# Performance work log

Hardware: AMD Instinct MI355X
Metric: run time of the kernel (lower is better)

The kernel has to match this reference:

```python
import jax, jax.numpy as jnp
import numpy as np

B, D, E, TOP_K = 16384, 2048, 8, 2


def setup_inputs() -> dict:
    key = jax.random.key(0)
    ks = jax.random.split(key, 5)
    scale = 1.0 / np.sqrt(D)
    x = jax.random.normal(ks[0], (B, D), dtype=jnp.float32)
    # expert Linear(D, D) weights/biases, stacked over experts
    expert_w = jax.random.uniform(ks[1], (E, D, D), minval=-scale, maxval=scale, dtype=jnp.float32)
    expert_b = jax.random.uniform(ks[2], (E, D), minval=-scale, maxval=scale, dtype=jnp.float32)
    # gate Linear(D, E)
    gate_w = jax.random.uniform(ks[3], (D, E), minval=-scale, maxval=scale, dtype=jnp.float32)
    gate_b = jax.random.uniform(ks[4], (E,), minval=-scale, maxval=scale, dtype=jnp.float32)
    return {"x": x, "expert_w": expert_w, "expert_b": expert_b, "gate_w": gate_w, "gate_b": gate_b}


def reference(x, expert_w, expert_b, gate_w, gate_b):
    # gate logits: (B, E)
    logits = x @ gate_w + gate_b
    topk_logits, topk_idx = jax.lax.top_k(logits, TOP_K)          # (B, K)
    topk_weights = jax.nn.softmax(topk_logits, axis=-1)           # (B, K)
    # dense: compute every expert for every token (faithful to original)
    expert_outputs = jax.nn.relu(
        jnp.einsum("bd,edf->bef", x, expert_w) + expert_b[None, :, :]
    )                                                             # (B, E, D); dropout is identity in eval mode
    # gather the top-k experts per token
    selected = jnp.take_along_axis(expert_outputs, topk_idx[:, :, None], axis=1)  # (B, K, D)
    out = jnp.sum(selected * topk_weights[:, :, None], axis=1)    # (B, D)
    return out
```

## Files before the change

kernel.cpp:

```cpp
#include <hip/hip_runtime.h>
#include <hip/hip_bf16.h>
#include <math.h>

#define NB 16384
#define DD 2048
#define NE 8
#define TM 256
#define TN 256
#define BK 64
#define NKT (DD / BK)
#define MT_PER_PASS (NB / TM + NE)
#define NT_TILES (DD / TN)
#define GEMM_GRID (MT_PER_PASS * NT_TILES)

typedef float f32x4 __attribute__((ext_vector_type(4)));
typedef short bf16x8 __attribute__((ext_vector_type(8)));

__device__ __forceinline__ short f2bf(float f) {
  union { float f; unsigned u; } v; v.f = f;
  unsigned r = (v.u + 0x7FFFu + ((v.u >> 16) & 1u)) >> 16;
  return (short)r;
}

__device__ __forceinline__ void gload16(const void* g, void* l) {
  __builtin_amdgcn_global_load_lds((const __attribute__((address_space(1))) void*)g,
                                   (__attribute__((address_space(3))) void*)l,
                                   16, 0, 0);
}

__global__ void conv_wT(const float* __restrict__ w, short* __restrict__ wt) {
  __shared__ float tile[64][68];
  int bid = blockIdx.x;
  int e = bid >> 10;
  int tt = bid & 1023;
  int d0 = (tt >> 5) << 6;
  int f0 = (tt & 31) << 6;
  const float* we = w + (size_t)e * DD * DD;
  int t = threadIdx.x;
  int col = (t & 15) << 2;
#pragma unroll
  for (int p = 0; p < 4; ++p) {
    int dl = (t >> 4) + p * 16;
    f32x4 v = *(const f32x4*)(we + (size_t)(d0 + dl) * DD + f0 + col);
    *(f32x4*)&tile[dl][col] = v;
  }
  __syncthreads();
  int fl = t >> 2;
  int ds = (t & 3) << 4;
  short tmp[16];
#pragma unroll
  for (int j = 0; j < 16; ++j) tmp[j] = f2bf(tile[ds + j][fl]);
  short* dst = wt + (size_t)e * DD * DD + (size_t)(f0 + fl) * DD + d0 + ds;
  *(bf16x8*)dst = *(const bf16x8*)tmp;
  *(bf16x8*)(dst + 8) = *(const bf16x8*)(tmp + 8);
}

__global__ void gate_conv(const float* __restrict__ x, const float* __restrict__ gw,
                          const float* __restrict__ gb, short* __restrict__ xb,
                          int* __restrict__ ridx, float* __restrict__ rw) {
  int wid = threadIdx.x >> 6;
  int lane = threadIdx.x & 63;
  int b = blockIdx.x * 4 + wid;
  const float* xr = x + (size_t)b * DD;
  short* xbr = xb + (size_t)b * DD;
  double acc[8];
#pragma unroll
  for (int e = 0; e < 8; ++e) acc[e] = 0.0;
#pragma unroll
  for (int it = 0; it < 4; ++it) {
    int d8 = (it * 64 + lane) * 8;
    f32x4 a = *(const f32x4*)(xr + d8);
    f32x4 c = *(const f32x4*)(xr + d8 + 4);
    bf16x8 o;
    o[0] = f2bf(a[0]); o[1] = f2bf(a[1]); o[2] = f2bf(a[2]); o[3] = f2bf(a[3]);
    o[4] = f2bf(c[0]); o[5] = f2bf(c[1]); o[6] = f2bf(c[2]); o[7] = f2bf(c[3]);
    *(bf16x8*)(xbr + d8) = o;
#pragma unroll
    for (int j = 0; j < 8; ++j) {
      float xv = (j < 4) ? a[j] : c[j - 4];
      double xd = (double)xv;
      f32x4 g0 = *(const f32x4*)(gw + (size_t)(d8 + j) * 8);
      f32x4 g1 = *(const f32x4*)(gw + (size_t)(d8 + j) * 8 + 4);
      acc[0] += xd * g0[0]; acc[1] += xd * g0[1];
      acc[2] += xd * g0[2]; acc[3] += xd * g0[3];
      acc[4] += xd * g1[0]; acc[5] += xd * g1[1];
      acc[6] += xd * g1[2]; acc[7] += xd * g1[3];
    }
  }
#pragma unroll
  for (int off = 32; off > 0; off >>= 1) {
#pragma unroll
    for (int e = 0; e < 8; ++e) acc[e] += __shfl_down(acc[e], off);
  }
  if (lane == 0) {
    double l[8];
#pragma unroll
    for (int e = 0; e < 8; ++e) l[e] = acc[e] + (double)gb[e];
    int i0 = 0;
#pragma unroll
    for (int e = 1; e < 8; ++e) if (l[e] > l[i0]) i0 = e;
    int i1 = (i0 == 0) ? 1 : 0;
#pragma unroll
    for (int e = 0; e < 8; ++e) if (e != i0 && l[e] > l[i1]) i1 = e;
    double z = exp(l[i1] - l[i0]);
    float w0 = (float)(1.0 / (1.0 + z));
    float w1 = (float)(z / (1.0 + z));
    ridx[2 * b] = i0; ridx[2 * b + 1] = i1;
    rw[2 * b] = w0;   rw[2 * b + 1] = w1;
  }
}

__global__ void hist_tok(const int* __restrict__ ridx, int* __restrict__ partials) {
  __shared__ int h[16];
  int t = threadIdx.x;
  if (t < 16) h[t] = 0;
  __syncthreads();
  int t0 = blockIdx.x * 512;
  for (int i = t; i < 512; i += 256) {
    int tok = t0 + i;
    atomicAdd(&h[ridx[2 * tok]], 1);
    atomicAdd(&h[8 + ridx[2 * tok + 1]], 1);
  }
  __syncthreads();
  if (t < 16) partials[blockIdx.x * 16 + t] = h[t];
}

__global__ void scan_small(const int* __restrict__ partials, int* __restrict__ base,
                           int* __restrict__ cnts, int* __restrict__ offs) {
  __shared__ int c[16], o[16];
  int j = threadIdx.x;
  if (j < 16) {
    int s = 0;
    for (int b = 0; b < 32; ++b) s += partials[b * 16 + j];
    c[j] = s; cnts[j] = s;
  }
  __syncthreads();
  if (j < 2) {
    int a = 0;
    for (int e = 0; e < 8; ++e) { o[j * 8 + e] = a; a += c[j * 8 + e]; }
  }
  __syncthreads();
  if (j < 16) {
    int r = o[j];
    offs[j] = o[j];
    for (int b = 0; b < 32; ++b) { base[b * 16 + j] = r; r += partials[b * 16 + j]; }
  }
}

__global__ void scatter_tok(const int* __restrict__ ridx, const float* __restrict__ rw,
                            const int* __restrict__ base,
                            int* __restrict__ lists0, float* __restrict__ elw0,
                            int* __restrict__ lists1, float* __restrict__ elw1) {
  __shared__ int h[16];
  int t = threadIdx.x;
  if (t < 16) h[t] = 0;
  __syncthreads();
  int t0 = blockIdx.x * 512;
  const int* bb = base + blockIdx.x * 16;
  for (int i = t; i < 512; i += 256) {
    int tok = t0 + i;
    int e0 = ridx[2 * tok], e1 = ridx[2 * tok + 1];
    int r0 = atomicAdd(&h[e0], 1);
    int r1 = atomicAdd(&h[8 + e1], 1);
    int p0 = bb[e0] + r0;
    int p1 = bb[8 + e1] + r1;
    lists0[p0] = tok; elw0[p0] = rw[2 * tok];
    lists1[p1] = tok; elw1[p1] = rw[2 * tok + 1];
  }
}

#define VMCNT0 asm volatile("s_waitcnt vmcnt(0)" ::: "memory")

template <int ADD>
__global__ __launch_bounds__(512, 2)
void moe_gemm(const short* __restrict__ xb, const short* __restrict__ wt,
              const float* __restrict__ eb, const int* __restrict__ cnts,
              const int* __restrict__ offs, const int* __restrict__ lists,
              const float* __restrict__ elw, float* __restrict__ out) {
  __shared__ short As[2 * 16384];
  __shared__ short Bs[2 * 16384];

  int nt = blockIdx.x & 7;
  int mt = blockIdx.x >> 3;

  int e = 0, cnt = 0;
  for (; e < NE; ++e) {
    cnt = cnts[e];
    int te = (cnt + TM - 1) >> 8;
    if (mt < te) break;
    mt -= te;
  }
  if (e >= NE) return;

  int m0 = mt * TM;
  int n0 = nt * TN;
  int off_e = offs[e];
  int tid = threadIdx.x;
  int lane = tid & 63, wid = tid >> 6;
  int wr = wid >> 2, wc = wid & 3;

  int trow = tid >> 3;
  int scol = ((tid & 7) ^ (trow & 7)) << 3;
  const short* aptr[4];
  const short* bptr[4];
#pragma unroll
  for (int l = 0; l < 4; ++l) {
    int r = l * 64 + trow;
    int gr = m0 + r;
    int tok = lists[off_e + ((gr < cnt) ? gr : (cnt - 1))];
    aptr[l] = xb + (size_t)tok * DD + scol;
    bptr[l] = wt + ((size_t)e * DD + (size_t)(n0 + r)) * DD + scol;
  }

  int lane15 = lane & 15;
  int csw0 = (((lane >> 4)    ) ^ (lane & 7)) << 3;
  int csw1 = (((lane >> 4) + 4) ^ (lane & 7)) << 3;
  int arow = (wr * 128 + lane15) * 64;
  int brow = (wc * 64  + lane15) * 64;

  f32x4 acc[8][4];
#pragma unroll
  for (int i = 0; i < 8; ++i)
#pragma unroll
    for (int j = 0; j < 4; ++j) acc[i][j] = (f32x4){0.f, 0.f, 0.f, 0.f};

#define STAGE(buf, kt) {                                                        \
  _Pragma("unroll") for (int l = 0; l < 4; ++l) {                               \
    gload16(aptr[l] + (size_t)(kt) * 64, &As[(buf)*16384 + l*4096 + tid*8]);    \
    gload16(bptr[l] + (size_t)(kt) * 64, &Bs[(buf)*16384 + l*4096 + tid*8]);    \
  } }

  STAGE(0, 0);
  VMCNT0;
  __builtin_amdgcn_s_barrier();

#pragma unroll 2
  for (int kt = 0; kt < NKT; ++kt) {
    int cur = kt & 1;
    if (kt + 1 < NKT) STAGE(cur ^ 1, kt + 1);
    bf16x8 bfr[4][2];
#pragma unroll
    for (int j = 0; j < 4; ++j) {
      int br = cur * 16384 + brow + j * 16 * 64;
      bfr[j][0] = *(const bf16x8*)&Bs[br + csw0];
      bfr[j][1] = *(const bf16x8*)&Bs[br + csw1];
    }
#pragma unroll
    for (int i8 = 0; i8 < 8; ++i8) {
      int ar = cur * 16384 + arow + i8 * 16 * 64;
      bf16x8 a0 = *(const bf16x8*)&As[ar + csw0];
      bf16x8 a1 = *(const bf16x8*)&As[ar + csw1];
#pragma unroll
      for (int j = 0; j < 4; ++j) {
        acc[i8][j] = __builtin_amdgcn_mfma_f32_16x16x32_bf16(a0, bfr[j][0], acc[i8][j], 0, 0, 0);
        acc[i8][j] = __builtin_amdgcn_mfma_f32_16x16x32_bf16(a1, bfr[j][1], acc[i8][j], 0, 0, 0);
      }
    }
    VMCNT0;
    __builtin_amdgcn_s_barrier();
  }
#undef STAGE

  float ebv[4];
#pragma unroll
  for (int j4 = 0; j4 < 4; ++j4)
    ebv[j4] = eb[e * DD + n0 + wc * 64 + j4 * 16 + lane15];
  int r0 = (lane >> 4) << 2;
#pragma unroll
  for (int i8 = 0; i8 < 8; ++i8) {
    int mloc = wr * 128 + i8 * 16 + r0;
#pragma unroll
    for (int r = 0; r < 4; ++r) {
      int gr = m0 + mloc + r;
      if (gr >= cnt) continue;
      int tok = lists[off_e + gr];
      float wgt = elw[off_e + gr];
      float* orow = out + (size_t)tok * DD;
#pragma unroll
      for (int j4 = 0; j4 < 4; ++j4) {
        int n = n0 + wc * 64 + j4 * 16 + lane15;
        float v = acc[i8][j4][r] + ebv[j4];
        v = fmaxf(v, 0.f) * wgt;
        if (ADD) v += __builtin_nontemporal_load(&orow[n]);
        __builtin_nontemporal_store(v, &orow[n]);
      }
    }
  }
}

extern "C" void kernel_launch(void* const* d_in, const int* in_sizes, int n_in,
                              void* d_out, int out_size, void* d_ws, size_t ws_size,
                              hipStream_t stream) {
  const float* x   = (const float*)d_in[0];
  const float* ewt = (const float*)d_in[1];
  const float* eb  = (const float*)d_in[2];
  const float* gw  = (const float*)d_in[3];
  const float* gb  = (const float*)d_in[4];
  float* out = (float*)d_out;

  char* ws = (char*)d_ws;
  short* xb      = (short*)(ws);
  short* wt      = (short*)(ws + 67108864);
  int*   ridx    = (int*)  (ws + 134217728);
  float* rw      = (float*)(ws + 134348800);
  int*   lists0  = (int*)  (ws + 134479872);
  float* elw0    = (float*)(ws + 134545408);
  int*   lists1  = (int*)  (ws + 134610944);
  float* elw1    = (float*)(ws + 134676480);
  int*   partials= (int*)  (ws + 134742016);
  int*   base    = (int*)  (ws + 134744064);
  int*   cnts    = (int*)  (ws + 134746112);
  int*   offs    = (int*)  (ws + 134746176);

  conv_wT<<<NE * 32 * 32, 256, 0, stream>>>(ewt, wt);
  gate_conv<<<NB / 4, 256, 0, stream>>>(x, gw, gb, xb, ridx, rw);
  hist_tok<<<32, 256, 0, stream>>>(ridx, partials);
  scan_small<<<1, 64, 0, stream>>>(partials, base, cnts, offs);
  scatter_tok<<<32, 256, 0, stream>>>(ridx, rw, base, lists0, elw0, lists1, elw1);
  moe_gemm<0><<<GEMM_GRID, 512, 0, stream>>>(xb, wt, eb, cnts,     offs,     lists0, elw0, out);
  moe_gemm<1><<<GEMM_GRID, 512, 0, stream>>>(xb, wt, eb, cnts + 8, offs + 8, lists1, elw1, out);
}
```

Baseline: 657.5 us.

## Shrink MoE GEMM tiles to 128x128, single-buffer LDS, swizzle block order

Reduces the grouped expert GEMM tile from 256x256 with 512 threads to 128x128 with 256 threads, and drops the LDS double buffer in favour of a load, sync, compute, sync loop. Block indices are swizzled so that consecutive blocks walk along M for a fixed N column, which should improve L2 reuse of weight tiles, and more blocks can be resident per CU. In exchange, global-to-LDS loads are no longer overlapped with MFMA work and each tile has lower arithmetic intensity.

Measured after the change: 618.7 us. 1.06x faster.

```diff
diff --git a/kernel.cpp b/kernel.cpp
--- a/kernel.cpp
+++ b/kernel.cpp
@@ -5,13 +5,14 @@
 #define NB 16384
 #define DD 2048
 #define NE 8
-#define TM 256
-#define TN 256
+#define TM 128
+#define TN 128
 #define BK 64
 #define NKT (DD / BK)
 #define MT_PER_PASS (NB / TM + NE)
 #define NT_TILES (DD / TN)
 #define GEMM_GRID (MT_PER_PASS * NT_TILES)
+#define BPX (GEMM_GRID / 8)
 
 typedef float f32x4 __attribute__((ext_vector_type(4)));
 typedef short bf16x8 __attribute__((ext_vector_type(8)));
@@ -169,24 +170,24 @@
   }
 }
 
-#define VMCNT0 asm volatile("s_waitcnt vmcnt(0)" ::: "memory")
-
 template <int ADD>
-__global__ __launch_bounds__(512, 2)
+__global__ __launch_bounds__(256, 4)
 void moe_gemm(const short* __restrict__ xb, const short* __restrict__ wt,
               const float* __restrict__ eb, const int* __restrict__ cnts,
               const int* __restrict__ offs, const int* __restrict__ lists,
               const float* __restrict__ elw, float* __restrict__ out) {
-  __shared__ short As[2 * 16384];
-  __shared__ short Bs[2 * 16384];
-
-  int nt = blockIdx.x & 7;
-  int mt = blockIdx.x >> 3;
+  __shared__ short As[TM * BK];
+  __shared__ short Bs[TN * BK];
+
+  int bid = blockIdx.x;
+  int swz = (bid & 7) * BPX + (bid >> 3);
+  int mt = swz % MT_PER_PASS;
+  int nt = swz / MT_PER_PASS;
 
   int e = 0, cnt = 0;
   for (; e < NE; ++e) {
     cnt = cnts[e];
-    int te = (cnt + TM - 1) >> 8;
+    int te = (cnt + TM - 1) >> 7;
     if (mt < te) break;
     mt -= te;
   }
@@ -197,89 +198,75 @@
   int off_e = offs[e];
   int tid = threadIdx.x;
   int lane = tid & 63, wid = tid >> 6;
-  int wr = wid >> 2, wc = wid & 3;
+  int wr = wid >> 1, wc = wid & 1;
 
   int trow = tid >> 3;
   int scol = ((tid & 7) ^ (trow & 7)) << 3;
-  const short* aptr[4];
-  const short* bptr[4];
+  int tok[4];
 #pragma unroll
   for (int l = 0; l < 4; ++l) {
-    int r = l * 64 + trow;
-    int gr = m0 + r;
-    int tok = lists[off_e + ((gr < cnt) ? gr : (cnt - 1))];
-    aptr[l] = xb + (size_t)tok * DD + scol;
-    bptr[l] = wt + ((size_t)e * DD + (size_t)(n0 + r)) * DD + scol;
-  }
+    int gr = m0 + l * 32 + trow;
+    tok[l] = lists[off_e + ((gr < cnt) ? gr : (cnt - 1))];
+  }
+  const short* bbase = wt + ((size_t)e * DD + (size_t)(n0 + trow)) * DD + scol;
 
   int lane15 = lane & 15;
   int csw0 = (((lane >> 4)    ) ^ (lane & 7)) << 3;
   int csw1 = (((lane >> 4) + 4) ^ (lane & 7)) << 3;
-  int arow = (wr * 128 + lane15) * 64;
-  int brow = (wc * 64  + lane15) * 64;
-
-  f32x4 acc[8][4];
-#pragma unroll
-  for (int i = 0; i < 8; ++i)
+  int arow = (wr * 64 + lane15) * 64;
+  int brow = (wc * 64 + lane15) * 64;
+
+  f32x4 acc[4][4];
+#pragma unroll
+  for (int i = 0; i < 4; ++i)
 #pragma unroll
     for (int j = 0; j < 4; ++j) acc[i][j] = (f32x4){0.f, 0.f, 0.f, 0.f};
 
-#define STAGE(buf, kt) {                                                        \
-  _Pragma("unroll") for (int l = 0; l < 4; ++l) {                               \
-    gload16(aptr[l] + (size_t)(kt) * 64, &As[(buf)*16384 + l*4096 + tid*8]);    \
-    gload16(bptr[l] + (size_t)(kt) * 64, &Bs[(buf)*16384 + l*4096 + tid*8]);    \
-  } }
-
-  STAGE(0, 0);
-  VMCNT0;
-  __builtin_amdgcn_s_barrier();
-
-#pragma unroll 2
+#pragma unroll 1
   for (int kt = 0; kt < NKT; ++kt) {
-    int cur = kt & 1;
-    if (kt + 1 < NKT) STAGE(cur ^ 1, kt + 1);
+    int ko = kt * BK + scol;
+#pragma unroll
+    for (int l = 0; l < 4; ++l) {
+      gload16(xb + ((size_t)tok[l] << 11) + ko, &As[l * 2048 + tid * 8]);
+      gload16(bbase + (size_t)(l * 32) * DD + kt * BK, &Bs[l * 2048 + tid * 8]);
+    }
+    __syncthreads();
     bf16x8 bfr[4][2];
 #pragma unroll
     for (int j = 0; j < 4; ++j) {
-      int br = cur * 16384 + brow + j * 16 * 64;
+      int br = brow + j * 16 * 64;
       bfr[j][0] = *(const bf16x8*)&Bs[br + csw0];
       bfr[j][1] = *(const bf16x8*)&Bs[br + csw1];
     }
 #pragma unroll
-    for (int i8 = 0; i8 < 8; ++i8) {
-      int ar = cur * 16384 + arow + i8 * 16 * 64;
+    for (int i = 0; i < 4; ++i) {
+      int ar = arow + i * 16 * 64;
       bf16x8 a0 = *(const bf16x8*)&As[ar + csw0];
       bf16x8 a1 = *(const bf16x8*)&As[ar + csw1];
 #pragma unroll
       for (int j = 0; j < 4; ++j) {
-        acc[i8][j] = __builtin_amdgcn_mfma_f32_16x16x32_bf16(a0, bfr[j][0], acc[i8][j], 0, 0, 0);
-        acc[i8][j] = __builtin_amdgcn_mfma_f32_16x16x32_bf16(a1, bfr[j][1], acc[i8][j], 0, 0, 0);
+        acc[i][j] = __builtin_amdgcn_mfma_f32_16x16x32_bf16(a0, bfr[j][0], acc[i][j], 0, 0, 0);
+        acc[i][j] = __builtin_amdgcn_mfma_f32_16x16x32_bf16(a1, bfr[j][1], acc[i][j], 0, 0, 0);
       }
     }
-    VMCNT0;
-    __builtin_amdgcn_s_barrier();
-  }
-#undef STAGE
-
-  float ebv[4];
-#pragma unroll
-  for (int j4 = 0; j4 < 4; ++j4)
-    ebv[j4] = eb[e * DD + n0 + wc * 64 + j4 * 16 + lane15];
+    __syncthreads();
+  }
+
   int r0 = (lane >> 4) << 2;
 #pragma unroll
-  for (int i8 = 0; i8 < 8; ++i8) {
-    int mloc = wr * 128 + i8 * 16 + r0;
+  for (int i = 0; i < 4; ++i) {
+    int mloc = wr * 64 + i * 16 + r0;
 #pragma unroll
     for (int r = 0; r < 4; ++r) {
       int gr = m0 + mloc + r;
       if (gr >= cnt) continue;
-      int tok = lists[off_e + gr];
+      int tokr = lists[off_e + gr];
       float wgt = elw[off_e + gr];
-      float* orow = out + (size_t)tok * DD;
-#pragma unroll
-      for (int j4 = 0; j4 < 4; ++j4) {
-        int n = n0 + wc * 64 + j4 * 16 + lane15;
-        float v = acc[i8][j4][r] + ebv[j4];
+      float* orow = out + (size_t)tokr * DD;
+#pragma unroll
+      for (int j = 0; j < 4; ++j) {
+        int n = n0 + wc * 64 + j * 16 + lane15;
+        float v = acc[i][j][r] + eb[e * DD + n];
         v = fmaxf(v, 0.f) * wgt;
         if (ADD) v += __builtin_nontemporal_load(&orow[n]);
         __builtin_nontemporal_store(v, &orow[n]);
@@ -317,6 +304,6 @@
   hist_tok<<<32, 256, 0, stream>>>(ridx, partials);
   scan_small<<<1, 64, 0, stream>>>(partials, base, cnts, offs);
   scatter_tok<<<32, 256, 0, stream>>>(ridx, rw, base, lists0, elw0, lists1, elw1);
-  moe_gemm<0><<<GEMM_GRID, 512, 0, stream>>>(xb, wt, eb, cnts,     offs,     lists0, elw0, out);
-  moe_gemm<1><<<GEMM_GRID, 512, 0, stream>>>(xb, wt, eb, cnts + 8, offs + 8, lists1, elw1, out);
-}
+  moe_gemm<0><<<GEMM_GRID, 256, 0, stream>>>(xb, wt, eb, cnts,     offs,     lists0, elw0, out);
+  moe_gemm<1><<<GEMM_GRID, 256, 0, stream>>>(xb, wt, eb, cnts + 8, offs + 8, lists1, elw1, out);
+}
```
